# Kernel tuning notes

Measured on AMD Instinct MI355X. Metric: run time of the kernel, lower is better.

## Reference

```python
import jax, jax.numpy as jnp
import numpy as np

N_NODES = 200000
N_EDGES = 200000
X_SIZE = 256
H_SIZE = 256


def setup_inputs() -> dict:
    key = jax.random.key(0)
    ks = jax.random.split(key, 8)
    s = 1.0 / np.sqrt(H_SIZE)
    return {
        "x": jax.random.normal(ks[0], (N_NODES, X_SIZE), jnp.float32),
        "h": jax.random.normal(ks[1], (N_NODES, H_SIZE), jnp.float32),
        "c": jax.random.normal(ks[2], (N_NODES, H_SIZE), jnp.float32),
        "W_iou": jax.random.normal(ks[3], (3 * H_SIZE, X_SIZE), jnp.float32) * s,
        "U_iou": jax.random.normal(ks[4], (3 * H_SIZE, H_SIZE), jnp.float32) * s,
        "b_iou": jnp.zeros((1, 3 * H_SIZE), jnp.float32),
        "U_f_w": jax.random.normal(ks[5], (H_SIZE, H_SIZE), jnp.float32) * s,
        "U_f_b": jnp.zeros((H_SIZE,), jnp.float32),
        "edge_src": jax.random.randint(ks[6], (N_EDGES,), 0, N_NODES, jnp.int32),
        "edge_dst": jax.random.randint(ks[7], (N_EDGES,), 0, N_NODES, jnp.int32),
    }


def reference(x, h, c, W_iou, U_iou, b_iou, U_f_w, U_f_b, edge_src, edge_dst):
    n = x.shape[0]
    # --- message + reduce (DGL mailbox flattened to edge list) ---
    h_child = h[edge_src]                                   # [E, H] gather
    c_child = c[edge_src]                                   # [E, H]
    f = jax.nn.sigmoid(h_child @ U_f_w.T + U_f_b)           # per-child forget gate
    h_tild = jax.ops.segment_sum(h_child, edge_dst, num_segments=n)      # sum_j h_j
    c_agg = jax.ops.segment_sum(f * c_child, edge_dst, num_segments=n)   # sum_j f_j*c_j
    # --- node iou: W_iou(x) (node data) + U_iou(h_tild) from reduce ---
    iou = x @ W_iou.T + h_tild @ U_iou.T + b_iou            # [N, 3H]
    # --- apply_node_func ---
    i, o, u = jnp.split(iou, 3, axis=1)
    i = jax.nn.sigmoid(i)
    o = jax.nn.sigmoid(o)
    u = jnp.tanh(u)
    c_new = i * u + c_agg
    h_new = o * jnp.tanh(c_new)
    return h_new, c_new
```

## Files before the change

### kernel.cpp

```cpp
#include <hip/hip_runtime.h>

#define NN 200000
#define NE 200000
#define HD 256

typedef __attribute__((ext_vector_type(8))) short short8;
typedef __attribute__((ext_vector_type(4))) short short4v;
typedef __attribute__((ext_vector_type(4))) float f32x4;

static __device__ __forceinline__ unsigned short f2bf(float f) {
  unsigned u = __float_as_uint(f);
  u = (u + 0x7FFFu + ((u >> 16) & 1u)) >> 16;
  return (unsigned short)u;
}
static __device__ __forceinline__ float bf2f(unsigned short u) {
  return __uint_as_float(((unsigned)u) << 16);
}
static __device__ __forceinline__ float sigmoidf_(float x) {
  return 1.0f / (1.0f + __expf(-x));
}
static __device__ __forceinline__ float tanhf_(float x) {
  return 2.0f / (1.0f + __expf(-2.0f * x)) - 1.0f;
}
static __device__ __forceinline__ void atomAddF(float* p, float v) {
  __hip_atomic_fetch_add(p, v, __ATOMIC_RELAXED, __HIP_MEMORY_SCOPE_AGENT);
}
static __device__ __forceinline__ int atomAddI(int* p, int v) {
  return __hip_atomic_fetch_add(p, v, __ATOMIC_RELAXED, __HIP_MEMORY_SCOPE_AGENT);
}

#if defined(__HIP_DEVICE_COMPILE__)
static __device__ __forceinline__ void gload_lds16(const void* g, void* l) {
  __builtin_amdgcn_global_load_lds(
      (const __attribute__((address_space(1))) void*)g,
      (__attribute__((address_space(3))) void*)l, 16, 0, 0);
}
#else
static __device__ __forceinline__ void gload_lds16(const void*, void*) {}
#endif

#define OFF_WFB    0u
#define OFF_BP     131072u
#define OFF_BPERM  917504u
#define OFF_ROWPTR 920576u
#define OFF_NEXT   1720832u
#define OFF_SLOT   2520832u
#define OFF_PSRC   3320832u
#define OFF_BSUM   4120832u
#define OFF_ZERO   4121856u
#define OFF_FC     4122880u
#define WS_NEED    106522880ull

__global__ __launch_bounds__(256) void prep_kernel(
    const float* __restrict__ Ufw, const float* __restrict__ Wiou,
    const float* __restrict__ Uiou, const float* __restrict__ biou,
    unsigned short* __restrict__ Wfb, unsigned short* __restrict__ Bp,
    float* __restrict__ bperm) {
  int idx = blockIdx.x * 256 + threadIdx.x;
  if (idx < 65536) {
    Wfb[idx] = f2bf(Ufw[idx]);
  } else if (idx < 458752) {
    int o = idx - 65536;
    int kc = o / 24576;
    int rem = o - kc * 24576;
    int tt = rem / 512;
    int rem2 = rem - tt * 512;
    int ln = rem2 >> 3, e = rem2 & 7;
    int cc = ln & 15, kgp = ln >> 4;
    int kk = kc * 32 + kgp * 8 + e;
    int g = tt % 3, tj = tt / 3;
    int orow = g * 256 + tj * 16 + cc;
    float v = (kk < 256) ? Wiou[orow * 256 + kk] : Uiou[orow * 256 + (kk - 256)];
    Bp[o] = f2bf(v);
  } else if (idx < 459520) {
    int j2 = idx - 458752;
    int T = j2 >> 4, cc = j2 & 15;
    int g = T % 3, tj = T / 3;
    bperm[j2] = biou[g * 256 + tj * 16 + cc];
  }
}

__global__ __launch_bounds__(256) void prep_fb_kernel(
    const float* __restrict__ Ufw, const float* __restrict__ Wiou,
    const float* __restrict__ Uiou, const float* __restrict__ biou,
    unsigned short* __restrict__ Wfb, unsigned short* __restrict__ Wioub,
    unsigned short* __restrict__ Uioub, float* __restrict__ bperm) {
  int idx = blockIdx.x * 256 + threadIdx.x;
  if (idx < 65536) {
    Wfb[idx] = f2bf(Ufw[idx]);
  } else if (idx < 262144) {
    int i2 = idx - 65536;
    int rp = i2 >> 8, k = i2 & 255;
    int T = rp >> 4, cc = rp & 15;
    int g = T % 3, tj = T / 3;
    Wioub[i2] = f2bf(Wiou[(g * 256 + tj * 16 + cc) * 256 + k]);
  } else if (idx < 458752) {
    int i2 = idx - 262144;
    int rp = i2 >> 8, k = i2 & 255;
    int T = rp >> 4, cc = rp & 15;
    int g = T % 3, tj = T / 3;
    Uioub[i2] = f2bf(Uiou[(g * 256 + tj * 16 + cc) * 256 + k]);
  } else if (idx < 459520) {
    int j2 = idx - 458752;
    int T = j2 >> 4, cc = j2 & 15;
    int g = T % 3, tj = T / 3;
    bperm[j2] = biou[g * 256 + tj * 16 + cc];
  }
}

__global__ __launch_bounds__(256) void hist_kernel(const int* __restrict__ edst,
                                                   int* __restrict__ cnt) {
  int e = blockIdx.x * 256 + threadIdx.x;
  if (e < NE) atomAddI(&cnt[edst[e]], 1);
}

__global__ __launch_bounds__(256) void scan_part(const int* __restrict__ cnt,
                                                 int* __restrict__ rp,
                                                 int* __restrict__ bsum) {
  __shared__ int sd[256];
  int t = threadIdx.x;
  int base = blockIdx.x * 1024 + t * 4;
  int v0 = (base + 0 < NN) ? cnt[base + 0] : 0;
  int v1 = (base + 1 < NN) ? cnt[base + 1] : 0;
  int v2 = (base + 2 < NN) ? cnt[base + 2] : 0;
  int v3 = (base + 3 < NN) ? cnt[base + 3] : 0;
  int s = v0 + v1 + v2 + v3;
  sd[t] = s;
  __syncthreads();
  for (int off = 1; off < 256; off <<= 1) {
    int add = (t >= off) ? sd[t - off] : 0;
    __syncthreads();
    sd[t] += add;
    __syncthreads();
  }
  int run = sd[t] - s;
  if (base + 0 < NN) rp[base + 0] = run; run += v0;
  if (base + 1 < NN) rp[base + 1] = run; run += v1;
  if (base + 2 < NN) rp[base + 2] = run; run += v2;
  if (base + 3 < NN) rp[base + 3] = run;
  if (t == 255) bsum[blockIdx.x] = sd[255];
}

__global__ __launch_bounds__(256) void scan_top(int* __restrict__ bsum,
                                                int* __restrict__ rp, int nb) {
  __shared__ int sd[256];
  int t = threadIdx.x;
  int v = (t < nb) ? bsum[t] : 0;
  sd[t] = v;
  __syncthreads();
  for (int off = 1; off < 256; off <<= 1) {
    int add = (t >= off) ? sd[t - off] : 0;
    __syncthreads();
    sd[t] += add;
    __syncthreads();
  }
  bsum[t] = sd[t] - v;
  if (t == 0) rp[NN] = NE;
}

__global__ __launch_bounds__(256) void scan_add(int* __restrict__ rp,
                                                const int* __restrict__ bsum,
                                                int* __restrict__ nxt) {
  int t = threadIdx.x;
  int base = blockIdx.x * 1024 + t * 4;
  int off = bsum[blockIdx.x];
#pragma unroll
  for (int j = 0; j < 4; ++j) {
    int i = base + j;
    if (i < NN) {
      int val = rp[i] + off;
      rp[i] = val;
      nxt[i] = val;
    }
  }
}

__global__ __launch_bounds__(256) void scatter_kernel(
    const int* __restrict__ esrc, const int* __restrict__ edst,
    int* __restrict__ nxt, int* __restrict__ slotArr, int* __restrict__ psrc) {
  int e = blockIdx.x * 256 + threadIdx.x;
  if (e < NE) {
    int d = edst[e];
    int pos = atomAddI(&nxt[d], 1);
    slotArr[e] = pos;
    psrc[pos] = esrc[e];
  }
}

#define F_AS 72
#define F_BS 72

__global__ __launch_bounds__(256) void edge_fc_kernel(
    const float* __restrict__ h, const float* __restrict__ c,
    const unsigned short* __restrict__ Wfb, const float* __restrict__ Ufb,
    const int* __restrict__ esrc, const int* __restrict__ slotArr,
    unsigned short* __restrict__ fcb) {
  __shared__ __align__(16) unsigned short Als[64 * F_AS];
  __shared__ __align__(16) unsigned short Bls[256 * F_BS];
  __shared__ int srcl[64], slotl[64];

  const int tid = threadIdx.x;
  const int e0 = blockIdx.x * 64;
  if (tid < 64) { srcl[tid] = esrc[e0 + tid]; slotl[tid] = slotArr[e0 + tid]; }
  __syncthreads();

  const int lane = tid & 63;
  const int wv = tid >> 6;
  const int wm = wv >> 1, wn = wv & 1;
  const int cbase = lane & 15;
  const int kg = lane >> 4;

  f32x4 acc[2][8];
#pragma unroll
  for (int i = 0; i < 2; ++i)
#pragma unroll
    for (int j = 0; j < 8; ++j) acc[i][j] = {0.f, 0.f, 0.f, 0.f};

  const int arow = tid >> 2;
  const int acg = tid & 3;
  const float* hrow = h + (size_t)srcl[arow] * HD;

  for (int kc = 0; kc < 4; ++kc) {
    const int k0 = kc * 64;
    const float4* s4 = (const float4*)(hrow + k0 + acg * 16);
    float4 q0 = s4[0], q1 = s4[1], q2 = s4[2], q3 = s4[3];
    short8 p0, p1;
    p0[0] = f2bf(q0.x); p0[1] = f2bf(q0.y); p0[2] = f2bf(q0.z); p0[3] = f2bf(q0.w);
    p0[4] = f2bf(q1.x); p0[5] = f2bf(q1.y); p0[6] = f2bf(q1.z); p0[7] = f2bf(q1.w);
    p1[0] = f2bf(q2.x); p1[1] = f2bf(q2.y); p1[2] = f2bf(q2.z); p1[3] = f2bf(q2.w);
    p1[4] = f2bf(q3.x); p1[5] = f2bf(q3.y); p1[6] = f2bf(q3.z); p1[7] = f2bf(q3.w);
    short8* ap = (short8*)&Als[arow * F_AS + acg * 16];
    ap[0] = p0; ap[1] = p1;
#pragma unroll
    for (int i = 0; i < 8; ++i) {
      int f = tid + 256 * i;
      int row = f >> 3, ch = f & 7;
      short8 vb = *(const short8*)(Wfb + row * 256 + k0 + ch * 8);
      *(short8*)&Bls[row * F_BS + ch * 8] = vb;
    }
    __syncthreads();
#pragma unroll
    for (int ks = 0; ks < 2; ++ks) {
      short8 a0 = *(const short8*)&Als[(wm * 32 + cbase) * F_AS + ks * 32 + kg * 8];
      short8 a1 = *(const short8*)&Als[(wm * 32 + 16 + cbase) * F_AS + ks * 32 + kg * 8];
#pragma unroll
      for (int nt = 0; nt < 8; ++nt) {
        short8 b = *(const short8*)&Bls[(wn * 128 + nt * 16 + cbase) * F_BS + ks * 32 + kg * 8];
        acc[0][nt] = __builtin_amdgcn_mfma_f32_16x16x32_bf16(a0, b, acc[0][nt], 0, 0, 0);
        acc[1][nt] = __builtin_amdgcn_mfma_f32_16x16x32_bf16(a1, b, acc[1][nt], 0, 0, 0);
      }
    }
    __syncthreads();
  }
  const int rsub = kg * 4;
#pragma unroll
  for (int nt = 0; nt < 8; ++nt) {
    const int coln = wn * 128 + nt * 16 + cbase;
    const float bias = Ufb[coln];
#pragma unroll
    for (int mt = 0; mt < 2; ++mt) {
#pragma unroll
      for (int j = 0; j < 4; ++j) {
        const int el = wm * 32 + mt * 16 + rsub + j;
        const float fg = sigmoidf_(acc[mt][nt][j] + bias);
        const float cv = c[(size_t)srcl[el] * HD + coln];
        fcb[(size_t)slotl[el] * HD + coln] = f2bf(fg * cv);
      }
    }
  }
}

__global__ __launch_bounds__(256) void gather_kernel(
    const float* __restrict__ h, const int* __restrict__ rp,
    const int* __restrict__ psrc, unsigned short* __restrict__ fcb,
    float* __restrict__ cagg) {
  const int tid = threadIdx.x;
  const int node = blockIdx.x * 32 + (tid >> 3);
  const int cg = tid & 7;
  const int s0 = rp[node], s1 = rp[node + 1];

  float hs[32], cs[32];
#pragma unroll
  for (int q = 0; q < 32; ++q) { hs[q] = 0.f; cs[q] = 0.f; }

  for (int s = s0; s < s1; ++s) {
    const int src = psrc[s];
    const float4* hp = (const float4*)(h + (size_t)src * HD + cg * 32);
    const short8* fp = (const short8*)(fcb + (size_t)s * HD + cg * 32);
#pragma unroll
    for (int q = 0; q < 8; ++q) {
      float4 v = hp[q];
      hs[4 * q + 0] += v.x; hs[4 * q + 1] += v.y;
      hs[4 * q + 2] += v.z; hs[4 * q + 3] += v.w;
    }
#pragma unroll
    for (int q = 0; q < 4; ++q) {
      short8 w = fp[q];
#pragma unroll
      for (int e = 0; e < 8; ++e) cs[8 * q + e] += bf2f((unsigned short)w[e]);
    }
  }
  float4* cp = (float4*)(cagg + (size_t)node * HD + cg * 32);
#pragma unroll
  for (int q = 0; q < 8; ++q) {
    float4 v = {cs[4 * q + 0], cs[4 * q + 1], cs[4 * q + 2], cs[4 * q + 3]};
    cp[q] = v;
  }
  if (s1 > s0) {
    short8* hd = (short8*)(fcb + (size_t)s0 * HD + cg * 32);
#pragma unroll
    for (int q = 0; q < 4; ++q) {
      short8 p;
#pragma unroll
      for (int e = 0; e < 8; ++e) p[e] = f2bf(hs[8 * q + e]);
      hd[q] = p;
    }
  }
}

__global__ __launch_bounds__(256) void iou_gemm4_kernel(
    const float* __restrict__ x, const unsigned short* __restrict__ Bp,
    const float* __restrict__ bperm, const int* __restrict__ rp,
    const unsigned short* __restrict__ fcb, const char* __restrict__ zpage,
    float* __restrict__ out) {
  __shared__ __align__(16) unsigned char Als[16384];
  __shared__ __align__(16) unsigned char Bls[12288];

  const int tid = threadIdx.x;
  const int lane = tid & 63;
  const int wv = tid >> 6;
  const int cbase = lane & 15;
  const int kg = lane >> 4;

  const int bid = blockIdx.x;
  const int rgrp = bid >> 2;
  const int nq = bid & 3;
  const int r0 = rgrp * 128;

  const int cI = lane & 7;
  const int rbase = wv * 8 + (lane >> 3);
  const int offX = (cI * 16) ^ ((rbase & 7) << 4);
  const char* xsrc[4];
#pragma unroll
  for (int i = 0; i < 4; ++i) {
    int rr = r0 + rbase + i * 32; if (rr > NN - 1) rr = NN - 1;
    xsrc[i] = (const char*)x + (size_t)rr * 1024 + offX;
  }
  const int cH = lane & 3;
  const char* hsrc[2];
#pragma unroll
  for (int i = 0; i < 2; ++i) {
    const int rl = i * 64 + wv * 16 + (lane >> 2);
    int rr = r0 + rl; if (rr > NN - 1) rr = NN - 1;
    const int s0 = rp[rr], s1 = rp[rr + 1];
    const char* base = (s1 > s0) ? (const char*)(fcb + (size_t)s0 * HD) : zpage;
    hsrc[i] = base + ((cH * 16) ^ ((rl & 3) << 4));
  }
  const char* bsrc = (const char*)Bp + (size_t)nq * 12288 + (wv * 64 + lane) * 16;

  f32x4 acc[2][12];
#pragma unroll
  for (int m = 0; m < 2; ++m)
#pragma unroll
    for (int t = 0; t < 12; ++t) acc[m][t] = {0.f, 0.f, 0.f, 0.f};

  const int frow0 = wv * 32 + cbase;
  const int swX = (frow0 & 7) << 4;
  const int swH = (frow0 & 3) << 4;

  for (int kc = 0; kc < 16; ++kc) {
#pragma unroll
    for (int i = 0; i < 3; ++i)
      gload_lds16(bsrc + (size_t)kc * 49152 + i * 4096,
                  Bls + i * 4096 + wv * 1024);
    if (kc < 8) {
#pragma unroll
      for (int i = 0; i < 4; ++i)
        gload_lds16(xsrc[i] + kc * 128, Als + i * 4096 + wv * 1024);
    } else {
#pragma unroll
      for (int i = 0; i < 2; ++i)
        gload_lds16(hsrc[i] + (kc - 8) * 64, Als + i * 4096 + wv * 1024);
    }
    __syncthreads();

    short8 a0, a1;
    if (kc < 8) {
      const unsigned char* ar0 = Als + frow0 * 128;
      const unsigned char* ar1 = Als + (frow0 + 16) * 128;
      float4 q0 = *(const float4*)(ar0 + ((kg * 32) ^ swX));
      float4 q1 = *(const float4*)(ar0 + ((kg * 32 + 16) ^ swX));
      float4 q2 = *(const float4*)(ar1 + ((kg * 32) ^ swX));
      float4 q3 = *(const float4*)(ar1 + ((kg * 32 + 16) ^ swX));
      a0[0] = f2bf(q0.x); a0[1] = f2bf(q0.y); a0[2] = f2bf(q0.z); a0[3] = f2bf(q0.w);
      a0[4] = f2bf(q1.x); a0[5] = f2bf(q1.y); a0[6] = f2bf(q1.z); a0[7] = f2bf(q1.w);
      a1[0] = f2bf(q2.x); a1[1] = f2bf(q2.y); a1[2] = f2bf(q2.z); a1[3] = f2bf(q2.w);
      a1[4] = f2bf(q3.x); a1[5] = f2bf(q3.y); a1[6] = f2bf(q3.z); a1[7] = f2bf(q3.w);
    } else {
      a0 = *(const short8*)(Als + frow0 * 64 + ((kg * 16) ^ swH));
      a1 = *(const short8*)(Als + (frow0 + 16) * 64 + ((kg * 16) ^ swH));
    }
#pragma unroll
    for (int tt = 0; tt < 12; ++tt) {
      short8 b = *(const short8*)(Bls + tt * 1024 + lane * 16);
      acc[0][tt] = __builtin_amdgcn_mfma_f32_16x16x32_bf16(a0, b, acc[0][tt], 0, 0, 0);
      acc[1][tt] = __builtin_amdgcn_mfma_f32_16x16x32_bf16(a1, b, acc[1][tt], 0, 0, 0);
    }
    __syncthreads();
  }

  float* outc = out + (size_t)NN * HD;
#pragma unroll
  for (int t3 = 0; t3 < 4; ++t3) {
    const int TT = nq * 12 + 3 * t3;
    const float bi = bperm[(TT + 0) * 16 + cbase];
    const float bo = bperm[(TT + 1) * 16 + cbase];
    const float bu = bperm[(TT + 2) * 16 + cbase];
    const int j = (nq * 4 + t3) * 16 + cbase;
#pragma unroll
    for (int mf = 0; mf < 2; ++mf) {
#pragma unroll
      for (int jr = 0; jr < 4; ++jr) {
        const int rl = wv * 32 + mf * 16 + kg * 4 + jr;
        const int gr = r0 + rl;
        if (gr < NN) {
          const size_t idx = (size_t)gr * HD + j;
          const float iv = sigmoidf_(acc[mf][3 * t3 + 0][jr] + bi);
          const float ov = sigmoidf_(acc[mf][3 * t3 + 1][jr] + bo);
          const float uv = tanhf_(acc[mf][3 * t3 + 2][jr] + bu);
          const float cn = iv * uv + outc[idx];
          out[idx] = ov * tanhf_(cn);
          outc[idx] = cn;
        }
      }
    }
  }
}

__global__ __launch_bounds__(256) void edge_kernel(
    const float* __restrict__ h, const float* __restrict__ c,
    const unsigned short* __restrict__ Wfb, const float* __restrict__ Ufb,
    const int* __restrict__ esrc, const int* __restrict__ edst,
    float* h_tild, float* c_agg) {
  __shared__ __align__(16) unsigned short Als[64 * F_AS];
  __shared__ __align__(16) unsigned short Bls[256 * F_BS];
  __shared__ int srcl[64], dstl[64];

  const int tid = threadIdx.x;
  const int e0 = blockIdx.x * 64;
  if (tid < 64) { srcl[tid] = esrc[e0 + tid]; dstl[tid] = edst[e0 + tid]; }
  __syncthreads();

  const int lane = tid & 63;
  const int wv = tid >> 6;
  const int wm = wv >> 1, wn = wv & 1;
  const int cbase = lane & 15;
  const int kg = lane >> 4;

  f32x4 acc[2][8];
#pragma unroll
  for (int i = 0; i < 2; ++i)
#pragma unroll
    for (int j = 0; j < 8; ++j) acc[i][j] = {0.f, 0.f, 0.f, 0.f};

  const int arow = tid >> 2;
  const int acg = tid & 3;
  const float* hrow = h + (size_t)srcl[arow] * HD;
  float* htrow = h_tild + (size_t)dstl[arow] * HD;

  for (int kc = 0; kc < 4; ++kc) {
    const int k0 = kc * 64;
    const float4* s4 = (const float4*)(hrow + k0 + acg * 16);
    float4 q0 = s4[0], q1 = s4[1], q2 = s4[2], q3 = s4[3];
    short8 p0, p1;
    p0[0] = f2bf(q0.x); p0[1] = f2bf(q0.y); p0[2] = f2bf(q0.z); p0[3] = f2bf(q0.w);
    p0[4] = f2bf(q1.x); p0[5] = f2bf(q1.y); p0[6] = f2bf(q1.z); p0[7] = f2bf(q1.w);
    p1[0] = f2bf(q2.x); p1[1] = f2bf(q2.y); p1[2] = f2bf(q2.z); p1[3] = f2bf(q2.w);
    p1[4] = f2bf(q3.x); p1[5] = f2bf(q3.y); p1[6] = f2bf(q3.z); p1[7] = f2bf(q3.w);
    short8* ap = (short8*)&Als[arow * F_AS + acg * 16];
    ap[0] = p0; ap[1] = p1;
    {
      float* hp = htrow + k0 + acg * 16;
      atomAddF(hp + 0, q0.x);  atomAddF(hp + 1, q0.y);
      atomAddF(hp + 2, q0.z);  atomAddF(hp + 3, q0.w);
      atomAddF(hp + 4, q1.x);  atomAddF(hp + 5, q1.y);
      atomAddF(hp + 6, q1.z);  atomAddF(hp + 7, q1.w);
      atomAddF(hp + 8, q2.x);  atomAddF(hp + 9, q2.y);
      atomAddF(hp + 10, q2.z); atomAddF(hp + 11, q2.w);
      atomAddF(hp + 12, q3.x); atomAddF(hp + 13, q3.y);
      atomAddF(hp + 14, q3.z); atomAddF(hp + 15, q3.w);
    }
#pragma unroll
    for (int i = 0; i < 8; ++i) {
      int f = tid + 256 * i;
      int row = f >> 3, ch = f & 7;
      short8 vb = *(const short8*)(Wfb + row * 256 + k0 + ch * 8);
      *(short8*)&Bls[row * F_BS + ch * 8] = vb;
    }
    __syncthreads();
#pragma unroll
    for (int ks = 0; ks < 2; ++ks) {
      short8 a0 = *(const short8*)&Als[(wm * 32 + cbase) * F_AS + ks * 32 + kg * 8];
      short8 a1 = *(const short8*)&Als[(wm * 32 + 16 + cbase) * F_AS + ks * 32 + kg * 8];
#pragma unroll
      for (int nt = 0; nt < 8; ++nt) {
        short8 b = *(const short8*)&Bls[(wn * 128 + nt * 16 + cbase) * F_BS + ks * 32 + kg * 8];
        acc[0][nt] = __builtin_amdgcn_mfma_f32_16x16x32_bf16(a0, b, acc[0][nt], 0, 0, 0);
        acc[1][nt] = __builtin_amdgcn_mfma_f32_16x16x32_bf16(a1, b, acc[1][nt], 0, 0, 0);
      }
    }
    __syncthreads();
  }
  const int rsub = kg * 4;
#pragma unroll
  for (int nt = 0; nt < 8; ++nt) {
    const int coln = wn * 128 + nt * 16 + cbase;
    const float bias = Ufb[coln];
#pragma unroll
    for (int mt = 0; mt < 2; ++mt) {
#pragma unroll
      for (int j = 0; j < 4; ++j) {
        const int el = wm * 32 + mt * 16 + rsub + j;
        const float fg = sigmoidf_(acc[mt][nt][j] + bias);
        const float cv = c[(size_t)srcl[el] * HD + coln];
        atomAddF(c_agg + (size_t)dstl[el] * HD + coln, fg * cv);
      }
    }
  }
}

#define I_AS 40
#define I_BS 40

__global__ __launch_bounds__(256) void iou_kernel(
    const float* __restrict__ x, const unsigned short* __restrict__ Wioub,
    const unsigned short* __restrict__ Uioub, const float* __restrict__ bperm,
    float* out) {
  __shared__ __align__(16) unsigned short Als[32 * I_AS];
  __shared__ __align__(16) unsigned short Bls[768 * I_BS];

  const int tid = threadIdx.x;
  const int lane = tid & 63;
  const int wv = tid >> 6;
  const int wm = wv >> 1, wn = wv & 1;
  const int cbase = lane & 15;
  const int kg = lane >> 4;
  const int r0 = blockIdx.x * 32;

  float* h_tild = out;
  float* c_agg = out + (size_t)NN * HD;

  f32x4 acc[24];
#pragma unroll
  for (int t = 0; t < 24; ++t) acc[t] = {0.f, 0.f, 0.f, 0.f};

  const int arow = tid >> 3;
  const int acg = tid & 7;

  for (int pass = 0; pass < 2; ++pass) {
    const float* As = pass ? h_tild : x;
    const unsigned short* Bs = pass ? Uioub : Wioub;
    for (int kc = 0; kc < 8; ++kc) {
      const int k0 = kc * 32;
      float4 q = *(const float4*)(As + (size_t)(r0 + arow) * HD + k0 + acg * 4);
      short4v p;
      p[0] = f2bf(q.x); p[1] = f2bf(q.y); p[2] = f2bf(q.z); p[3] = f2bf(q.w);
      *(short4v*)&Als[arow * I_AS + acg * 4] = p;
#pragma unroll
      for (int i = 0; i < 12; ++i) {
        int f = tid + 256 * i;
        int row = f >> 2, ch = f & 3;
        short8 vb = *(const short8*)(Bs + row * 256 + k0 + ch * 8);
        *(short8*)&Bls[row * I_BS + ch * 8] = vb;
      }
      __syncthreads();
      short8 a = *(const short8*)&Als[(wm * 16 + cbase) * I_AS + kg * 8];
#pragma unroll
      for (int tt = 0; tt < 24; ++tt) {
        short8 b = *(const short8*)&Bls[((wn * 24 + tt) * 16 + cbase) * I_BS + kg * 8];
        acc[tt] = __builtin_amdgcn_mfma_f32_16x16x32_bf16(a, b, acc[tt], 0, 0, 0);
      }
      __syncthreads();
    }
  }
  const int rsub = kg * 4;
#pragma unroll
  for (int t3 = 0; t3 < 8; ++t3) {
    const int T = wn * 24 + 3 * t3;
    const float bi = bperm[(T + 0) * 16 + cbase];
    const float bo = bperm[(T + 1) * 16 + cbase];
    const float bu = bperm[(T + 2) * 16 + cbase];
    const int j = (wn * 8 + t3) * 16 + cbase;
#pragma unroll
    for (int jr = 0; jr < 4; ++jr) {
      const int r = r0 + wm * 16 + rsub + jr;
      const size_t idx = (size_t)r * HD + j;
      const float iv = sigmoidf_(acc[3 * t3 + 0][jr] + bi);
      const float ov = sigmoidf_(acc[3 * t3 + 1][jr] + bo);
      const float uv = tanhf_(acc[3 * t3 + 2][jr] + bu);
      const float cn = iv * uv + c_agg[idx];
      out[idx] = ov * tanhf_(cn);
      c_agg[idx] = cn;
    }
  }
}

extern "C" void kernel_launch(void* const* d_in, const int* in_sizes, int n_in,
                              void* d_out, int out_size, void* d_ws, size_t ws_size,
                              hipStream_t stream) {
  const float* x    = (const float*)d_in[0];
  const float* h    = (const float*)d_in[1];
  const float* c    = (const float*)d_in[2];
  const float* Wiou = (const float*)d_in[3];
  const float* Uiou = (const float*)d_in[4];
  const float* biou = (const float*)d_in[5];
  const float* Ufw  = (const float*)d_in[6];
  const float* Ufb  = (const float*)d_in[7];
  const int* esrc   = (const int*)d_in[8];
  const int* edst   = (const int*)d_in[9];
  float* out = (float*)d_out;

  char* ws = (char*)d_ws;
  unsigned short* Wfb   = (unsigned short*)(ws + OFF_WFB);
  unsigned short* Bp    = (unsigned short*)(ws + OFF_BP);
  float* bperm          = (float*)(ws + OFF_BPERM);

  if (ws_size >= WS_NEED) {
    int* rpp  = (int*)(ws + OFF_ROWPTR);
    int* nxt  = (int*)(ws + OFF_NEXT);
    int* slot = (int*)(ws + OFF_SLOT);
    int* psrc = (int*)(ws + OFF_PSRC);
    int* bsum = (int*)(ws + OFF_BSUM);
    char* zpage = ws + OFF_ZERO;
    unsigned short* fcb = (unsigned short*)(ws + OFF_FC);

    (void)hipMemsetAsync(nxt, 0, (size_t)NN * sizeof(int), stream);
    (void)hipMemsetAsync(zpage, 0, 1024, stream);
    prep_kernel<<<1795, 256, 0, stream>>>(Ufw, Wiou, Uiou, biou, Wfb, Bp, bperm);
    hist_kernel<<<(NE + 255) / 256, 256, 0, stream>>>(edst, nxt);
    scan_part<<<(NN + 1023) / 1024, 256, 0, stream>>>(nxt, rpp, bsum);
    scan_top<<<1, 256, 0, stream>>>(bsum, rpp, (NN + 1023) / 1024);
    scan_add<<<(NN + 1023) / 1024, 256, 0, stream>>>(rpp, bsum, nxt);
    scatter_kernel<<<(NE + 255) / 256, 256, 0, stream>>>(esrc, edst, nxt, slot, psrc);
    edge_fc_kernel<<<NE / 64, 256, 0, stream>>>(h, c, Wfb, Ufb, esrc, slot, fcb);
    gather_kernel<<<NN / 32, 256, 0, stream>>>(h, rpp, psrc, fcb, out + (size_t)NN * HD);
    const int rgrps = (NN + 127) / 128;
    iou_gemm4_kernel<<<rgrps * 4, 256, 0, stream>>>(x, Bp, bperm, rpp, fcb, zpage, out);
  } else {
    unsigned short* Wioub = (unsigned short*)(ws + OFF_BP);
    unsigned short* Uioub = (unsigned short*)(ws + OFF_BP + 393216);
    (void)hipMemsetAsync(d_out, 0, (size_t)out_size * sizeof(float), stream);
    prep_fb_kernel<<<1795, 256, 0, stream>>>(Ufw, Wiou, Uiou, biou, Wfb, Wioub, Uioub, bperm);
    edge_kernel<<<NE / 64, 256, 0, stream>>>(h, c, Wfb, Ufb, esrc, edst,
                                             out, out + (size_t)NN * HD);
    iou_kernel<<<NN / 32, 256, 0, stream>>>(x, Wioub, Uioub, bperm, out);
  }
}
```

Before: 870.5 us.

## Retile IOU GEMM to 8 column groups with deeper K chunks

The IOU GEMM now splits the output columns into 8 groups instead of 4, halving accumulators per thread, and each block processes 64-wide K chunks so there are 8 iterations instead of 16. This halves the number of barriers and lets the kernel target 3 blocks per CU. The fp32-to-bf16 conversion of x now truncates by taking the high halves with a byte-permute instead of rounding to nearest, which trades a little precision for fewer ALU ops. Splitting into 8 column groups means each x row tile is reloaded from global memory twice as often.

```diff
diff --git a/kernel.cpp b/kernel.cpp
--- a/kernel.cpp
+++ b/kernel.cpp
@@ -7,6 +7,7 @@
 typedef __attribute__((ext_vector_type(8))) short short8;
 typedef __attribute__((ext_vector_type(4))) short short4v;
 typedef __attribute__((ext_vector_type(4))) float f32x4;
+typedef __attribute__((ext_vector_type(4))) unsigned int u32x4;
 
 static __device__ __forceinline__ unsigned short f2bf(float f) {
   unsigned u = __float_as_uint(f);
@@ -35,8 +36,14 @@
       (const __attribute__((address_space(1))) void*)g,
       (__attribute__((address_space(3))) void*)l, 16, 0, 0);
 }
+static __device__ __forceinline__ unsigned pack_hi16(unsigned lo, unsigned hi) {
+  return __builtin_amdgcn_perm(hi, lo, 0x07060302u);
+}
 #else
 static __device__ __forceinline__ void gload_lds16(const void*, void*) {}
+static __device__ __forceinline__ unsigned pack_hi16(unsigned lo, unsigned hi) {
+  return (lo >> 16) | (hi & 0xffff0000u);
+}
 #endif
 
 #define OFF_WFB    0u
@@ -318,12 +325,12 @@
   }
 }
 
-__global__ __launch_bounds__(256) void iou_gemm4_kernel(
+__global__ __launch_bounds__(256, 3) void iou_gemm5_kernel(
     const float* __restrict__ x, const unsigned short* __restrict__ Bp,
     const float* __restrict__ bperm, const int* __restrict__ rp,
     const unsigned short* __restrict__ fcb, const char* __restrict__ zpage,
     float* __restrict__ out) {
-  __shared__ __align__(16) unsigned char Als[16384];
+  __shared__ __align__(16) unsigned char Als[32768];
   __shared__ __align__(16) unsigned char Bls[12288];
 
   const int tid = threadIdx.x;
@@ -333,96 +340,125 @@
   const int kg = lane >> 4;
 
   const int bid = blockIdx.x;
-  const int rgrp = bid >> 2;
-  const int nq = bid & 3;
-  const int r0 = rgrp * 128;
-
-  const int cI = lane & 7;
-  const int rbase = wv * 8 + (lane >> 3);
-  const int offX = (cI * 16) ^ ((rbase & 7) << 4);
-  const char* xsrc[4];
+  const int cg = bid & 7;
+  const int r0 = (bid >> 3) * 128;
+  const bool full = (r0 + 128 <= NN);
+
+  const unsigned xswz = ((unsigned)(tid & 15) * 16) ^ ((((unsigned)(tid >> 4)) & 7) << 5);
+  const char* xbase = (const char*)x + (size_t)(full ? (r0 + (tid >> 4)) : (NN - 1)) * 1024 + xswz;
+
+  const unsigned hswz = ((unsigned)(tid & 7) * 16) ^ ((((unsigned)(tid >> 3)) & 7) << 4);
+  const char* hsrc[4];
 #pragma unroll
   for (int i = 0; i < 4; ++i) {
-    int rr = r0 + rbase + i * 32; if (rr > NN - 1) rr = NN - 1;
-    xsrc[i] = (const char*)x + (size_t)rr * 1024 + offX;
-  }
-  const int cH = lane & 3;
-  const char* hsrc[2];
-#pragma unroll
-  for (int i = 0; i < 2; ++i) {
-    const int rl = i * 64 + wv * 16 + (lane >> 2);
-    int rr = r0 + rl; if (rr > NN - 1) rr = NN - 1;
+    int rr = r0 + i * 32 + (tid >> 3);
+    if (rr >= NN) rr = NN - 1;
     const int s0 = rp[rr], s1 = rp[rr + 1];
     const char* base = (s1 > s0) ? (const char*)(fcb + (size_t)s0 * HD) : zpage;
-    hsrc[i] = base + ((cH * 16) ^ ((rl & 3) << 4));
-  }
-  const char* bsrc = (const char*)Bp + (size_t)nq * 12288 + (wv * 64 + lane) * 16;
-
-  f32x4 acc[2][12];
+    hsrc[i] = base + hswz;
+  }
+
+  f32x4 acc[2][6];
 #pragma unroll
   for (int m = 0; m < 2; ++m)
 #pragma unroll
-    for (int t = 0; t < 12; ++t) acc[m][t] = {0.f, 0.f, 0.f, 0.f};
+    for (int t = 0; t < 6; ++t) acc[m][t] = {0.f, 0.f, 0.f, 0.f};
 
   const int frow0 = wv * 32 + cbase;
-  const int swX = (frow0 & 7) << 4;
-  const int swH = (frow0 & 3) << 4;
-
-  for (int kc = 0; kc < 16; ++kc) {
-#pragma unroll
-    for (int i = 0; i < 3; ++i)
-      gload_lds16(bsrc + (size_t)kc * 49152 + i * 4096,
-                  Bls + i * 4096 + wv * 1024);
-    if (kc < 8) {
-#pragma unroll
-      for (int i = 0; i < 4; ++i)
-        gload_lds16(xsrc[i] + kc * 128, Als + i * 4096 + wv * 1024);
+  const unsigned swx = ((unsigned)(frow0 & 7)) << 5;
+  const unsigned swh = ((unsigned)(frow0 & 7)) << 4;
+  const unsigned char* ar0x = Als + frow0 * 256;
+  const unsigned char* ar1x = Als + (frow0 + 16) * 256;
+  const unsigned char* ar0h = Als + frow0 * 128;
+  const unsigned char* ar1h = Als + (frow0 + 16) * 128;
+  unsigned char* lA = Als + wv * 1024 + lane * 16;
+  unsigned char* lB = Bls + wv * 1024 + lane * 16;
+  const unsigned char* bread = Bls + lane * 16;
+
+  for (int kc = 0; kc < 4; ++kc) {
+#pragma unroll
+    for (int i = 0; i < 3; ++i) {
+      const int f = i * 4 + wv;
+      const int kch = f / 6, t = f - kch * 6;
+      gload_lds16((const char*)Bp + ((size_t)(kc * 2 + kch) * 48 + cg * 6 + t) * 1024 + lane * 16,
+                  lB + i * 4096);
+    }
+    if (full) {
+#pragma unroll
+      for (int i = 0; i < 8; ++i)
+        gload_lds16(xbase + (size_t)i * 16384 + kc * 256, lA + i * 4096);
     } else {
 #pragma unroll
-      for (int i = 0; i < 2; ++i)
-        gload_lds16(hsrc[i] + (kc - 8) * 64, Als + i * 4096 + wv * 1024);
-    }
-    __syncthreads();
-
-    short8 a0, a1;
-    if (kc < 8) {
-      const unsigned char* ar0 = Als + frow0 * 128;
-      const unsigned char* ar1 = Als + (frow0 + 16) * 128;
-      float4 q0 = *(const float4*)(ar0 + ((kg * 32) ^ swX));
-      float4 q1 = *(const float4*)(ar0 + ((kg * 32 + 16) ^ swX));
-      float4 q2 = *(const float4*)(ar1 + ((kg * 32) ^ swX));
-      float4 q3 = *(const float4*)(ar1 + ((kg * 32 + 16) ^ swX));
-      a0[0] = f2bf(q0.x); a0[1] = f2bf(q0.y); a0[2] = f2bf(q0.z); a0[3] = f2bf(q0.w);
-      a0[4] = f2bf(q1.x); a0[5] = f2bf(q1.y); a0[6] = f2bf(q1.z); a0[7] = f2bf(q1.w);
-      a1[0] = f2bf(q2.x); a1[1] = f2bf(q2.y); a1[2] = f2bf(q2.z); a1[3] = f2bf(q2.w);
-      a1[4] = f2bf(q3.x); a1[5] = f2bf(q3.y); a1[6] = f2bf(q3.z); a1[7] = f2bf(q3.w);
-    } else {
-      a0 = *(const short8*)(Als + frow0 * 64 + ((kg * 16) ^ swH));
-      a1 = *(const short8*)(Als + (frow0 + 16) * 64 + ((kg * 16) ^ swH));
-    }
-#pragma unroll
-    for (int tt = 0; tt < 12; ++tt) {
-      short8 b = *(const short8*)(Bls + tt * 1024 + lane * 16);
-      acc[0][tt] = __builtin_amdgcn_mfma_f32_16x16x32_bf16(a0, b, acc[0][tt], 0, 0, 0);
-      acc[1][tt] = __builtin_amdgcn_mfma_f32_16x16x32_bf16(a1, b, acc[1][tt], 0, 0, 0);
+      for (int i = 0; i < 8; ++i) {
+        int rr = r0 + i * 16 + (tid >> 4);
+        if (rr >= NN) rr = NN - 1;
+        gload_lds16((const char*)x + (size_t)rr * 1024 + kc * 256 + xswz, lA + i * 4096);
+      }
+    }
+    __syncthreads();
+#pragma unroll
+    for (int ks = 0; ks < 2; ++ks) {
+      u32x4 q0 = *(const u32x4*)(ar0x + ((unsigned)(ks * 128 + kg * 32) ^ swx));
+      u32x4 q1 = *(const u32x4*)(ar0x + ((unsigned)(ks * 128 + kg * 32 + 16) ^ swx));
+      u32x4 q2 = *(const u32x4*)(ar1x + ((unsigned)(ks * 128 + kg * 32) ^ swx));
+      u32x4 q3 = *(const u32x4*)(ar1x + ((unsigned)(ks * 128 + kg * 32 + 16) ^ swx));
+      u32x4 p0, p1;
+      p0[0] = pack_hi16(q0[0], q0[1]); p0[1] = pack_hi16(q0[2], q0[3]);
+      p0[2] = pack_hi16(q1[0], q1[1]); p0[3] = pack_hi16(q1[2], q1[3]);
+      p1[0] = pack_hi16(q2[0], q2[1]); p1[1] = pack_hi16(q2[2], q2[3]);
+      p1[2] = pack_hi16(q3[0], q3[1]); p1[3] = pack_hi16(q3[2], q3[3]);
+      short8 a0 = __builtin_bit_cast(short8, p0);
+      short8 a1 = __builtin_bit_cast(short8, p1);
+#pragma unroll
+      for (int t = 0; t < 6; ++t) {
+        short8 b = *(const short8*)(bread + (ks * 6 + t) * 1024);
+        acc[0][t] = __builtin_amdgcn_mfma_f32_16x16x32_bf16(a0, b, acc[0][t], 0, 0, 0);
+        acc[1][t] = __builtin_amdgcn_mfma_f32_16x16x32_bf16(a1, b, acc[1][t], 0, 0, 0);
+      }
+    }
+    __syncthreads();
+  }
+
+  for (int kc = 4; kc < 8; ++kc) {
+#pragma unroll
+    for (int i = 0; i < 3; ++i) {
+      const int f = i * 4 + wv;
+      const int kch = f / 6, t = f - kch * 6;
+      gload_lds16((const char*)Bp + ((size_t)(kc * 2 + kch) * 48 + cg * 6 + t) * 1024 + lane * 16,
+                  lB + i * 4096);
+    }
+    const int kcH = kc - 4;
+#pragma unroll
+    for (int i = 0; i < 4; ++i)
+      gload_lds16(hsrc[i] + kcH * 128, lA + i * 4096);
+    __syncthreads();
+#pragma unroll
+    for (int ks = 0; ks < 2; ++ks) {
+      short8 a0 = *(const short8*)(ar0h + ((unsigned)(ks * 64 + kg * 16) ^ swh));
+      short8 a1 = *(const short8*)(ar1h + ((unsigned)(ks * 64 + kg * 16) ^ swh));
+#pragma unroll
+      for (int t = 0; t < 6; ++t) {
+        short8 b = *(const short8*)(bread + (ks * 6 + t) * 1024);
+        acc[0][t] = __builtin_amdgcn_mfma_f32_16x16x32_bf16(a0, b, acc[0][t], 0, 0, 0);
+        acc[1][t] = __builtin_amdgcn_mfma_f32_16x16x32_bf16(a1, b, acc[1][t], 0, 0, 0);
+      }
     }
     __syncthreads();
   }
 
   float* outc = out + (size_t)NN * HD;
 #pragma unroll
-  for (int t3 = 0; t3 < 4; ++t3) {
-    const int TT = nq * 12 + 3 * t3;
+  for (int t3 = 0; t3 < 2; ++t3) {
+    const int TT = cg * 6 + 3 * t3;
     const float bi = bperm[(TT + 0) * 16 + cbase];
     const float bo = bperm[(TT + 1) * 16 + cbase];
     const float bu = bperm[(TT + 2) * 16 + cbase];
-    const int j = (nq * 4 + t3) * 16 + cbase;
+    const int j = (cg * 2 + t3) * 16 + cbase;
 #pragma unroll
     for (int mf = 0; mf < 2; ++mf) {
 #pragma unroll
       for (int jr = 0; jr < 4; ++jr) {
-        const int rl = wv * 32 + mf * 16 + kg * 4 + jr;
-        const int gr = r0 + rl;
+        const int gr = r0 + wv * 32 + mf * 16 + kg * 4 + jr;
         if (gr < NN) {
           const size_t idx = (size_t)gr * HD + j;
           const float iv = sigmoidf_(acc[mf][3 * t3 + 0][jr] + bi);
@@ -645,7 +681,7 @@
     edge_fc_kernel<<<NE / 64, 256, 0, stream>>>(h, c, Wfb, Ufb, esrc, slot, fcb);
     gather_kernel<<<NN / 32, 256, 0, stream>>>(h, rpp, psrc, fcb, out + (size_t)NN * HD);
     const int rgrps = (NN + 127) / 128;
-    iou_gemm4_kernel<<<rgrps * 4, 256, 0, stream>>>(x, Bp, bperm, rpp, fcb, zpage, out);
+    iou_gemm5_kernel<<<rgrps * 8, 256, 0, stream>>>(x, Bp, bperm, rpp, fcb, zpage, out);
   } else {
     unsigned short* Wioub = (unsigned short*)(ws + OFF_BP);
     unsigned short* Uioub = (unsigned short*)(ws + OFF_BP + 393216);
```

New measurement: 835.2 us. 1.04x faster.
